# Kernel tuning notes

Hardware: AMD Instinct MI355X
Metric: run time of the kernel (lower is better)

## Reference

```python
import jax, jax.numpy as jnp
import numpy as np

B, L, D, K = 8, 4096, 1024, 2048  # batch, seq_len, hidden, max selected tokens


def setup_inputs() -> dict:
    key = jax.random.key(0)
    k1, k2 = jax.random.split(key)
    hidden_states = jax.random.normal(k1, (B, L, D), dtype=jnp.float32)
    # boundary_mask with exactly K True per row so next_max_seqlen == K is static
    scores = jax.random.uniform(k2, (B, L))
    order = jnp.argsort(scores, axis=1)  # random permutation per row
    boundary_mask = jnp.zeros((B, L), dtype=bool)
    rows = jnp.arange(B)[:, None]
    boundary_mask = boundary_mask.at[rows, order[:, :K]].set(True)
    mask = jnp.ones((B, L), dtype=bool)
    return {
        "hidden_states": hidden_states,
        "boundary_mask": boundary_mask,
        "mask": mask,
        "next_max_seqlen": K,
    }


def reference(hidden_states, boundary_mask, mask, next_max_seqlen):
    # Padded path of ChunkLayer.forward (mask is provided, cu_seqlens=None).
    Bn, Ln, Dn = hidden_states.shape
    num_tokens = boundary_mask.sum(axis=-1)  # [B]
    # boundary tokens keep their position; non-boundary tokens pushed past L
    token_idx = jnp.arange(Ln)[None, :] + (~boundary_mask).astype(jnp.int32) * Ln
    seq_sorted_indices = jnp.argsort(token_idx, axis=1)  # stable sort, [B, L]
    idx = seq_sorted_indices[:, :next_max_seqlen, None]  # [B, K, 1]
    next_hidden_states = jnp.take_along_axis(hidden_states, idx, axis=1)  # [B, K, D]
    next_mask = jnp.arange(next_max_seqlen)[None, :] < num_tokens[:, None]  # [B, K]
    return next_hidden_states, next_mask
```

## Files before the change

### kernel.cpp

```cpp
#include <hip/hip_runtime.h>

#define BB 8
#define LL 4096
#define DD 1024
#define KK 2048

__global__ void build_idx_kernel(const int* __restrict__ bm,
                                 int* __restrict__ idx,
                                 float* __restrict__ om) {
    __shared__ int wsum[16];
    const int b    = blockIdx.x;
    const int tid  = threadIdx.x;
    const int lane = tid & 63;
    const int wave = tid >> 6;

    const int* m = bm + (size_t)b * LL;

    const int base = tid * 4;
    const int4 v = *reinterpret_cast<const int4*>(m + base);
    int local[4] = { v.x != 0, v.y != 0, v.z != 0, v.w != 0 };
    const int s = local[0] + local[1] + local[2] + local[3];

    int incl = s;
#pragma unroll
    for (int off = 1; off < 64; off <<= 1) {
        const int t = __shfl_up(incl, off, 64);
        if (lane >= off) incl += t;
    }
    if (lane == 63) wsum[wave] = incl;
    __syncthreads();

    if (wave == 0) {
        int wv = (lane < 16) ? wsum[lane] : 0;
#pragma unroll
        for (int off = 1; off < 16; off <<= 1) {
            const int t = __shfl_up(wv, off, 64);
            if (lane >= off) wv += t;
        }
        if (lane < 16) wsum[lane] = wv;
    }
    __syncthreads();

    const int total   = wsum[15];
    const int waveoff = (wave == 0) ? 0 : wsum[wave - 1];
    int brank = waveoff + incl - s;

    int* ib = idx + (size_t)b * KK;
#pragma unroll
    for (int j = 0; j < 4; ++j) {
        const int i = base + j;
        if (local[j]) {
            if (brank < KK) ib[brank] = i;
            ++brank;
        } else {
            const int nr = total + (i - brank);
            if (nr < KK) ib[nr] = i;
        }
    }

    float* omb = om + (size_t)b * KK;
    omb[tid]        = (tid        < total) ? 1.0f : 0.0f;
    omb[tid + 1024] = (tid + 1024 < total) ? 1.0f : 0.0f;
}

__global__ void __launch_bounds__(256)
gather_kernel(const float4* __restrict__ src,
              const int* __restrict__ idx,
              float4* __restrict__ dst) {
    const int row  = blockIdx.x;
    const int b    = row >> 11;
    const int srow = idx[row];
    const float4* s = src + ((size_t)b * LL + srow) * (DD / 4);
    float4*       d = dst + (size_t)row * (DD / 4);
    d[threadIdx.x] = s[threadIdx.x];
}

extern "C" void kernel_launch(void* const* d_in, const int* in_sizes, int n_in,
                              void* d_out, int out_size, void* d_ws, size_t ws_size,
                              hipStream_t stream) {
    const float* hs = (const float*)d_in[0];
    const int*   bm = (const int*)d_in[1];

    float* out_hs   = (float*)d_out;
    float* out_mask = (float*)d_out + (size_t)BB * KK * DD;

    int* idx = (int*)d_ws;

    build_idx_kernel<<<BB, 1024, 0, stream>>>(bm, idx, out_mask);
    gather_kernel<<<BB * KK, DD / 4, 0, stream>>>((const float4*)hs, idx, (float4*)out_hs);
}
```

Baseline: 29.47 us.

## Fuse index build into gather with per-block ballot bitmask rank select

Merges the index-building kernel into the gather kernel. Each block redundantly rebuilds its batch row's boundary bitmask with wave ballots, takes a prefix sum over 64 words, and binary-searches plus popcount-selects the source row for its 8 output rows. Each block then copies 8 rows with nontemporal loads and stores. This drops one kernel launch and the idx round-trip through global memory, but every block rereads the 16KB mask row and repeats the scan.

```diff
diff --git a/kernel.cpp b/kernel.cpp
--- a/kernel.cpp
+++ b/kernel.cpp
@@ -5,74 +5,85 @@
 #define DD 1024
 #define KK 2048
 
-__global__ void build_idx_kernel(const int* __restrict__ bm,
-                                 int* __restrict__ idx,
-                                 float* __restrict__ om) {
-    __shared__ int wsum[16];
-    const int b    = blockIdx.x;
-    const int tid  = threadIdx.x;
-    const int lane = tid & 63;
-    const int wave = tid >> 6;
+#define RPB 8
+#define NWORDS (LL / 64)
+
+typedef float f32x4 __attribute__((ext_vector_type(4)));
+
+__global__ void __launch_bounds__(256)
+fused_gather_kernel(const f32x4* __restrict__ src,
+                    const int* __restrict__ bm,
+                    f32x4* __restrict__ dst,
+                    float* __restrict__ om) {
+    __shared__ unsigned long long words[NWORDS];
+    __shared__ int pre[NWORDS];
+    __shared__ int srows[RPB];
+
+    const int blk   = blockIdx.x;
+    const int tid   = threadIdx.x;
+    const int lane  = tid & 63;
+    const int wave  = tid >> 6;
+    const int b     = blk >> 8;
+    const int kbase = (blk & 255) * RPB;
 
     const int* m = bm + (size_t)b * LL;
 
-    const int base = tid * 4;
-    const int4 v = *reinterpret_cast<const int4*>(m + base);
-    int local[4] = { v.x != 0, v.y != 0, v.z != 0, v.w != 0 };
-    const int s = local[0] + local[1] + local[2] + local[3];
-
-    int incl = s;
 #pragma unroll
-    for (int off = 1; off < 64; off <<= 1) {
-        const int t = __shfl_up(incl, off, 64);
-        if (lane >= off) incl += t;
+    for (int j = 0; j < 16; ++j) {
+        const unsigned long long w = __ballot(m[j * 256 + tid] != 0);
+        if (lane == 0) {
+            const int wi = j * 4 + wave;
+            words[wi] = w;
+            pre[wi]   = __popcll(w);
+        }
     }
-    if (lane == 63) wsum[wave] = incl;
     __syncthreads();
 
     if (wave == 0) {
-        int wv = (lane < 16) ? wsum[lane] : 0;
+        int v = pre[lane];
 #pragma unroll
-        for (int off = 1; off < 16; off <<= 1) {
-            const int t = __shfl_up(wv, off, 64);
-            if (lane >= off) wv += t;
+        for (int off = 1; off < 64; off <<= 1) {
+            const int t = __shfl_up(v, off, 64);
+            if (lane >= off) v += t;
         }
-        if (lane < 16) wsum[lane] = wv;
+        pre[lane] = v;
     }
     __syncthreads();
 
-    const int total   = wsum[15];
-    const int waveoff = (wave == 0) ? 0 : wsum[wave - 1];
-    int brank = waveoff + incl - s;
+    const int total = pre[NWORDS - 1];
 
-    int* ib = idx + (size_t)b * KK;
+    if (tid < RPB) {
+        const int kb = kbase + tid;
+        int lo = 0, hi = NWORDS - 1, r;
+        unsigned long long x;
+        if (kb < total) {
+            while (lo < hi) { const int mid = (lo + hi) >> 1; if (pre[mid] > kb) hi = mid; else lo = mid + 1; }
+            r = kb - ((lo == 0) ? 0 : pre[lo - 1]);
+            x = words[lo];
+        } else {
+            const int rz = kb - total;
+            while (lo < hi) { const int mid = (lo + hi) >> 1; if ((mid + 1) * 64 - pre[mid] > rz) hi = mid; else lo = mid + 1; }
+            r = rz - (lo * 64 - ((lo == 0) ? 0 : pre[lo - 1]));
+            x = ~words[lo];
+        }
+        int pos = 0;
 #pragma unroll
-    for (int j = 0; j < 4; ++j) {
-        const int i = base + j;
-        if (local[j]) {
-            if (brank < KK) ib[brank] = i;
-            ++brank;
-        } else {
-            const int nr = total + (i - brank);
-            if (nr < KK) ib[nr] = i;
+        for (int sh = 32; sh >= 1; sh >>= 1) {
+            const int c = __popcll(x & ((1ull << sh) - 1ull));
+            if (r >= c) { r -= c; x >>= sh; pos += sh; }
         }
+        srows[tid] = lo * 64 + pos;
+        om[(size_t)b * KK + kb] = (kb < total) ? 1.0f : 0.0f;
     }
+    __syncthreads();
 
-    float* omb = om + (size_t)b * KK;
-    omb[tid]        = (tid        < total) ? 1.0f : 0.0f;
-    omb[tid + 1024] = (tid + 1024 < total) ? 1.0f : 0.0f;
-}
-
-__global__ void __launch_bounds__(256)
-gather_kernel(const float4* __restrict__ src,
-              const int* __restrict__ idx,
-              float4* __restrict__ dst) {
-    const int row  = blockIdx.x;
-    const int b    = row >> 11;
-    const int srow = idx[row];
-    const float4* s = src + ((size_t)b * LL + srow) * (DD / 4);
-    float4*       d = dst + (size_t)row * (DD / 4);
-    d[threadIdx.x] = s[threadIdx.x];
+    const size_t srcbase = (size_t)b * LL * (DD / 4);
+    const size_t dstbase = ((size_t)b * KK + kbase) * (DD / 4);
+#pragma unroll
+    for (int j = 0; j < RPB; ++j) {
+        const f32x4 v = __builtin_nontemporal_load(&src[srcbase + (size_t)srows[j] * (DD / 4) + tid]);
+        __builtin_nontemporal_store(v, &dst[dstbase + (size_t)j * (DD / 4) + tid]);
+    }
 }
 
 extern "C" void kernel_launch(void* const* d_in, const int* in_sizes, int n_in,
@@ -84,8 +95,6 @@
     float* out_hs   = (float*)d_out;
     float* out_mask = (float*)d_out + (size_t)BB * KK * DD;
 
-    int* idx = (int*)d_ws;
-
-    build_idx_kernel<<<BB, 1024, 0, stream>>>(bm, idx, out_mask);
-    gather_kernel<<<BB * KK, DD / 4, 0, stream>>>((const float4*)hs, idx, (float4*)out_hs);
+    fused_gather_kernel<<<(BB * KK) / RPB, 256, 0, stream>>>(
+        (const f32x4*)hs, bm, (f32x4*)out_hs, out_mask);
 }
```

New measurement: 29.20 us. Within noise of the previous version (-0.9%).
